# Kernel tuning notes

Hardware: AMD Instinct MI355X
Metric: run time of the kernel (lower is better)

The kernel has to match this reference:

```python
import jax, jax.numpy as jnp
import numpy as np

N_NODES = 100000
N_GRAPHS = 64
NEG_SLOPE = 0.2  # PyG GATConv default leaky_relu slope


def gat_conv(x, src, dst, W, a_src, a_dst, b, heads, out_c, concat, num_nodes):
    # x: [N, F_in]; W: [heads*out_c, F_in]; a_src/a_dst: [heads, out_c]
    h = (x @ W.T).reshape(num_nodes, heads, out_c)            # [N, H, C]
    s_src = jnp.sum(h * a_src, axis=-1)                       # [N, H]
    s_dst = jnp.sum(h * a_dst, axis=-1)                       # [N, H]
    e = jax.nn.leaky_relu(s_src[src] + s_dst[dst], NEG_SLOPE)  # [E, H]
    # segment softmax over incoming edges of each destination node
    m = jax.ops.segment_max(e, dst, num_segments=num_nodes)   # [N, H]
    m = jnp.where(jnp.isfinite(m), m, 0.0)
    e = jnp.exp(e - m[dst])
    denom = jax.ops.segment_sum(e, dst, num_segments=num_nodes)  # [N, H]
    alpha = e / (denom[dst] + 1e-16)                           # [E, H]
    msg = alpha[:, :, None] * h[src]                           # [E, H, C]
    out = jax.ops.segment_sum(msg, dst, num_segments=num_nodes)  # [N, H, C]
    if concat:
        out = out.reshape(num_nodes, heads * out_c)
    else:
        out = out.mean(axis=1)
    return out + b


def setup_inputs() -> dict:
    key = jax.random.key(0)
    ks = jax.random.split(key, 12)
    x = jax.random.normal(ks[0], (N_NODES, 128), dtype=jnp.float32)
    edge_index = jax.random.randint(ks[1], (2, 1600000), 0, N_NODES, dtype=jnp.int64)
    batch = jnp.sort(jax.random.randint(ks[2], (N_NODES,), 0, N_GRAPHS, dtype=jnp.int64))
    # conv1: 128 -> 16, heads=4, concat -> 64
    W1 = jax.random.normal(ks[3], (64, 128), dtype=jnp.float32) * 0.1
    att_src1 = jax.random.normal(ks[4], (4, 16), dtype=jnp.float32) * 0.1
    att_dst1 = jax.random.normal(ks[5], (4, 16), dtype=jnp.float32) * 0.1
    b1 = jnp.zeros((64,), dtype=jnp.float32)
    # conv2: 64 -> 10, heads=1, concat=False
    W2 = jax.random.normal(ks[6], (10, 64), dtype=jnp.float32) * 0.1
    att_src2 = jax.random.normal(ks[7], (1, 10), dtype=jnp.float32) * 0.1
    att_dst2 = jax.random.normal(ks[8], (1, 10), dtype=jnp.float32) * 0.1
    b2 = jnp.zeros((10,), dtype=jnp.float32)
    return {"x": x, "edge_index": edge_index, "batch": batch,
            "W1": W1, "att_src1": att_src1, "att_dst1": att_dst1, "b1": b1,
            "W2": W2, "att_src2": att_src2, "att_dst2": att_dst2, "b2": b2}


def reference(x, edge_index, batch, W1, att_src1, att_dst1, b1, W2, att_src2, att_dst2, b2):
    N = x.shape[0]
    # PyG GATConv adds self-loops by default
    loop = jnp.arange(N, dtype=edge_index.dtype)
    src = jnp.concatenate([edge_index[0], loop])
    dst = jnp.concatenate([edge_index[1], loop])
    # dropout layers are inactive in eval mode
    h = gat_conv(x, src, dst, W1, att_src1, att_dst1, b1, heads=4, out_c=16, concat=True, num_nodes=N)
    h = jax.nn.elu(h)
    h = gat_conv(h, src, dst, W2, att_src2, att_dst2, b2, heads=1, out_c=10, concat=False, num_nodes=N)
    # global_mean_pool over graphs in the batch
    sums = jax.ops.segment_sum(h, batch, num_segments=N_GRAPHS)
    counts = jax.ops.segment_sum(jnp.ones((N,), dtype=h.dtype), batch, num_segments=N_GRAPHS)
    pooled = sums / jnp.maximum(counts, 1.0)[:, None]
    return jax.nn.log_softmax(pooled, axis=1)
```

## Files before the change

kernel.cpp:

```cpp
#include <hip/hip_runtime.h>
#include <hip/hip_bf16.h>
#include <math.h>

#define BSHIFT 7
#define BWIDTH (1 << BSHIFT)
#define BCAP 2560
#define A3_TILE 4096

typedef float floatx2 __attribute__((ext_vector_type(2)));
typedef __attribute__((ext_vector_type(8))) short bf16x8;
typedef __attribute__((ext_vector_type(4))) float f32x4;

__device__ inline unsigned int f2bf(float f) {
    unsigned int u = __float_as_uint(f);
    return (u + 0x7FFFu + ((u >> 16) & 1u)) >> 16;
}
__device__ inline float bflo(unsigned int u) { return __uint_as_float(u << 16); }
__device__ inline float bfhi(unsigned int u) { return __uint_as_float(u & 0xFFFF0000u); }

__device__ inline void fp8x16_fma2(uint4 Wv, float we, floatx2* q) {
    floatx2 w2; w2[0] = we; w2[1] = we;
    q[0] += w2 * __builtin_amdgcn_cvt_pk_f32_fp8((int)Wv.x, false);
    q[1] += w2 * __builtin_amdgcn_cvt_pk_f32_fp8((int)Wv.x, true);
    q[2] += w2 * __builtin_amdgcn_cvt_pk_f32_fp8((int)Wv.y, false);
    q[3] += w2 * __builtin_amdgcn_cvt_pk_f32_fp8((int)Wv.y, true);
    q[4] += w2 * __builtin_amdgcn_cvt_pk_f32_fp8((int)Wv.z, false);
    q[5] += w2 * __builtin_amdgcn_cvt_pk_f32_fp8((int)Wv.z, true);
    q[6] += w2 * __builtin_amdgcn_cvt_pk_f32_fp8((int)Wv.w, false);
    q[7] += w2 * __builtin_amdgcn_cvt_pk_f32_fp8((int)Wv.w, true);
}

#define G1_BM 128

__device__ void gemm1_body(char* smem, int bid,
    const float* __restrict__ x, const float* __restrict__ W1,
    const float* __restrict__ a_src, const float* __restrict__ a_dst,
    unsigned char* __restrict__ h1f, float* __restrict__ s1s,
    float* __restrict__ s1d, int N)
{
    unsigned short (*xb)[136] = (unsigned short(*)[136])smem;
    unsigned short (*wb)[136] = (unsigned short(*)[136])(smem + 34816);
    float (*hls)[68] = (float(*)[68])smem;

    int tid = threadIdx.x;
    int nb = bid * G1_BM;

    #pragma unroll
    for (int r = 0; r < 8; ++r) {
        int i = tid + r * 256;
        int ch = i >> 5, kq = i & 31;
        float4 v = *(const float4*)&W1[ch * 128 + kq * 4];
        uint2 pk;
        pk.x = f2bf(v.x) | (f2bf(v.y) << 16);
        pk.y = f2bf(v.z) | (f2bf(v.w) << 16);
        *(uint2*)&wb[ch][kq * 4] = pk;
    }
    #pragma unroll
    for (int r = 0; r < 16; ++r) {
        int i = tid + r * 256;
        int nl = i >> 5, kq = i & 31;
        int n = nb + nl;
        float4 v = (n < N) ? *(const float4*)&x[(size_t)n * 128 + kq * 4]
                           : make_float4(0.f, 0.f, 0.f, 0.f);
        uint2 pk;
        pk.x = f2bf(v.x) | (f2bf(v.y) << 16);
        pk.y = f2bf(v.z) | (f2bf(v.w) << 16);
        *(uint2*)&xb[nl][kq * 4] = pk;
    }
    __syncthreads();

    int lane = tid & 63, wv = tid >> 6;
    int lr = lane & 15, lk = lane >> 4;
    f32x4 acc[2][4];
    #pragma unroll
    for (int mt = 0; mt < 2; ++mt)
        #pragma unroll
        for (int nt = 0; nt < 4; ++nt) acc[mt][nt] = (f32x4){0.f, 0.f, 0.f, 0.f};

    #pragma unroll
    for (int ks = 0; ks < 4; ++ks) {
        int k0 = ks * 32 + lk * 8;
        bf16x8 af0 = *(const bf16x8*)&xb[wv * 32 + lr][k0];
        bf16x8 af1 = *(const bf16x8*)&xb[wv * 32 + 16 + lr][k0];
        #pragma unroll
        for (int nt = 0; nt < 4; ++nt) {
            bf16x8 bf = *(const bf16x8*)&wb[nt * 16 + lr][k0];
            acc[0][nt] = __builtin_amdgcn_mfma_f32_16x16x32_bf16(af0, bf, acc[0][nt], 0, 0, 0);
            acc[1][nt] = __builtin_amdgcn_mfma_f32_16x16x32_bf16(af1, bf, acc[1][nt], 0, 0, 0);
        }
    }
    __syncthreads();
    #pragma unroll
    for (int mt = 0; mt < 2; ++mt)
        #pragma unroll
        for (int nt = 0; nt < 4; ++nt)
            #pragma unroll
            for (int reg = 0; reg < 4; ++reg)
                hls[wv * 32 + mt * 16 + lk * 4 + reg][nt * 16 + lr] = acc[mt][nt][reg];
    __syncthreads();

    int nl = tid >> 1, half = tid & 1;
    int n = nb + nl;
    if (n < N) {
        float v[32];
        #pragma unroll
        for (int q = 0; q < 8; ++q) {
            float4 t4 = *(const float4*)&hls[nl][half * 32 + q * 4];
            v[q*4+0] = t4.x; v[q*4+1] = t4.y; v[q*4+2] = t4.z; v[q*4+3] = t4.w;
        }
        int h0 = half * 2, h1 = half * 2 + 1;
        float ss0 = 0.f, sd0 = 0.f, ss1 = 0.f, sd1 = 0.f;
        #pragma unroll
        for (int j = 0; j < 16; ++j) {
            ss0 += v[j] * a_src[h0 * 16 + j];
            sd0 += v[j] * a_dst[h0 * 16 + j];
            ss1 += v[16 + j] * a_src[h1 * 16 + j];
            sd1 += v[16 + j] * a_dst[h1 * 16 + j];
        }
        s1s[n * 4 + h0] = ss0; s1d[n * 4 + h0] = sd0;
        s1s[n * 4 + h1] = ss1; s1d[n * 4 + h1] = sd1;

        unsigned int w0, w1v, w2v, w3v, w4v, w5v, w6v, w7v;
        w0  = (unsigned)__builtin_amdgcn_cvt_pk_fp8_f32(v[0],  v[1],  0, false);
        w0  = (unsigned)__builtin_amdgcn_cvt_pk_fp8_f32(v[2],  v[3],  (int)w0, true);
        w1v = (unsigned)__builtin_amdgcn_cvt_pk_fp8_f32(v[4],  v[5],  0, false);
        w1v = (unsigned)__builtin_amdgcn_cvt_pk_fp8_f32(v[6],  v[7],  (int)w1v, true);
        w2v = (unsigned)__builtin_amdgcn_cvt_pk_fp8_f32(v[8],  v[9],  0, false);
        w2v = (unsigned)__builtin_amdgcn_cvt_pk_fp8_f32(v[10], v[11], (int)w2v, true);
        w3v = (unsigned)__builtin_amdgcn_cvt_pk_fp8_f32(v[12], v[13], 0, false);
        w3v = (unsigned)__builtin_amdgcn_cvt_pk_fp8_f32(v[14], v[15], (int)w3v, true);
        w4v = (unsigned)__builtin_amdgcn_cvt_pk_fp8_f32(v[16], v[17], 0, false);
        w4v = (unsigned)__builtin_amdgcn_cvt_pk_fp8_f32(v[18], v[19], (int)w4v, true);
        w5v = (unsigned)__builtin_amdgcn_cvt_pk_fp8_f32(v[20], v[21], 0, false);
        w5v = (unsigned)__builtin_amdgcn_cvt_pk_fp8_f32(v[22], v[23], (int)w5v, true);
        w6v = (unsigned)__builtin_amdgcn_cvt_pk_fp8_f32(v[24], v[25], 0, false);
        w6v = (unsigned)__builtin_amdgcn_cvt_pk_fp8_f32(v[26], v[27], (int)w6v, true);
        w7v = (unsigned)__builtin_amdgcn_cvt_pk_fp8_f32(v[28], v[29], 0, false);
        w7v = (unsigned)__builtin_amdgcn_cvt_pk_fp8_f32(v[30], v[31], (int)w7v, true);
        *(uint4*)(h1f + (size_t)n * 64 + half * 32)      = make_uint4(w0, w1v, w2v, w3v);
        *(uint4*)(h1f + (size_t)n * 64 + half * 32 + 16) = make_uint4(w4v, w5v, w6v, w7v);
    }
}

__device__ void partition_body(char* smem, int bid,
    const int* __restrict__ ei, int* __restrict__ bcnt, int* __restrict__ pairs,
    int E, int NBK)
{
    int* hist       = (int*)smem;
    int* scanb      = hist + 1024;
    int* gbase      = scanb + 1024;
    int* partial    = gbase + 1024;
    int* stage_pack = partial + 256;
    int* stage_pos  = stage_pack + A3_TILE;

    int t = threadIdx.x;
    int e0 = bid * A3_TILE;
    for (int i = t; i < 1024; i += 256) hist[i] = 0;
    __syncthreads();
    int my_b[16], my_rank[16], my_pack[16];
    #pragma unroll
    for (int j = 0; j < 16; ++j) {
        int e = e0 + j * 256 + t;
        int b = -1, pack = 0, r = 0;
        if (e < E) {
            int s = ei[e], d = ei[E + e];
            b = d >> BSHIFT;
            pack = ((d & (BWIDTH - 1)) << 17) | s;
            r = atomicAdd(&hist[b], 1);
        }
        my_b[j] = b; my_pack[j] = pack; my_rank[j] = r;
    }
    __syncthreads();
    int b4 = t * 4;
    int h0 = hist[b4], h1v = hist[b4 + 1], h2v = hist[b4 + 2], h3v = hist[b4 + 3];
    int tot = h0 + h1v + h2v + h3v;
    partial[t] = tot;
    __syncthreads();
    for (int o = 1; o < 256; o <<= 1) {
        int u = (t >= o) ? partial[t - o] : 0;
        __syncthreads();
        partial[t] += u;
        __syncthreads();
    }
    int excl = partial[t] - tot;
    scanb[b4]     = excl;
    scanb[b4 + 1] = excl + h0;
    scanb[b4 + 2] = excl + h0 + h1v;
    scanb[b4 + 3] = excl + h0 + h1v + h2v;
    int nvalid = partial[255];
    for (int b = t; b < NBK; b += 256) {
        int c = hist[b];
        if (c > 0) gbase[b] = b * BCAP + atomicAdd(&bcnt[b], c);
    }
    __syncthreads();
    #pragma unroll
    for (int j = 0; j < 16; ++j) {
        int b = my_b[j];
        if (b >= 0) {
            int slot = scanb[b] + my_rank[j];
            stage_pack[slot] = my_pack[j];
            stage_pos[slot]  = gbase[b] + my_rank[j];
        }
    }
    __syncthreads();
    for (int i = t; i < nvalid; i += 256)
        pairs[stage_pos[i]] = stage_pack[i];
}

__global__ __launch_bounds__(256) void gp_kernel(
    const float* __restrict__ x, const float* __restrict__ W1,
    const float* __restrict__ a_src, const float* __restrict__ a_dst,
    unsigned char* __restrict__ h1f, float* __restrict__ s1s,
    float* __restrict__ s1d, const int* __restrict__ ei,
    int* __restrict__ bcnt, int* __restrict__ pairs,
    int N, int E, int NBK, int G1B)
{
    __shared__ __align__(16) char smem[52224];
    if ((int)blockIdx.x < G1B)
        gemm1_body(smem, blockIdx.x, x, W1, a_src, a_dst, h1f, s1s, s1d, N);
    else
        partition_body(smem, blockIdx.x - G1B, ei, bcnt, pairs, E, NBK);
}

__global__ __launch_bounds__(256) void buildcsr_kernel(
    const int* __restrict__ pairs, const int* __restrict__ bcnt,
    int* __restrict__ csr_src, int* __restrict__ meta, int N)
{
    int b = blockIdx.x;
    __shared__ int stage[BCAP];
    __shared__ int hist[BWIDTH];
    __shared__ int scn[BWIDTH];
    __shared__ int cur[BWIDTH];
    int t = threadIdx.x;
    if (t < BWIDTH) hist[t] = 0;
    __syncthreads();
    int cnt = bcnt[b];
    int base = b * BCAP;
    for (int i = t; i < cnt; i += 256) {
        int p = pairs[base + i];
        stage[i] = p;
        atomicAdd(&hist[(p >> 17) & (BWIDTH - 1)], 1);
    }
    __syncthreads();
    int v = (t < BWIDTH) ? hist[t] : 0;
    if (t < BWIDTH) scn[t] = v;
    __syncthreads();
    for (int o = 1; o < BWIDTH; o <<= 1) {
        int u = (t < BWIDTH && t >= o) ? scn[t - o] : 0;
        __syncthreads();
        if (t < BWIDTH) scn[t] += u;
        __syncthreads();
    }
    if (t < BWIDTH) {
        int excl = scn[t] - v;
        cur[t] = excl;
        int dst = b * BWIDTH + t;
        if (dst < N) meta[dst] = (excl << 16) | v;
    }
    __syncthreads();
    for (int i = t; i < cnt; i += 256) {
        int p = stage[i];
        int slot = atomicAdd(&cur[(p >> 17) & (BWIDTH - 1)], 1);
        csr_src[base + slot] = p & 0x1FFFF;
    }
}

__global__ __launch_bounds__(256) void agg1_kernel(
    const int* __restrict__ meta, const int* __restrict__ csr_src,
    const unsigned char* __restrict__ h1f, const float* __restrict__ s1s,
    const float* __restrict__ s1d, const float* __restrict__ b1,
    const float* __restrict__ W2, const float* __restrict__ as2,
    const float* __restrict__ ad2, unsigned short* __restrict__ h2p, int N)
{
    __shared__ float w2s[640];
    for (int i = threadIdx.x; i < 640; i += 256) w2s[i] = W2[i];
    __syncthreads();

    int tid = blockIdx.x * 256 + threadIdx.x;
    int n = tid >> 4, h = tid & 3, sub = (tid >> 2) & 3;
    floatx2 xq[8];
    #pragma unroll
    for (int j = 0; j < 8; ++j) { xq[j][0] = 0.f; xq[j][1] = 0.f; }
    float den = 0.f;

    if (n < N) {
        float sdst = s1d[n * 4 + h];
        if (sub == 0) {
            float s = s1s[n * 4 + h] + sdst;
            s = (s >= 0.f) ? s : 0.2f * s;
            float w = __expf(s);
            den = w;
            uint4 Wv = *(const uint4*)(h1f + ((size_t)n << 6) + (h << 4));
            fp8x16_fma2(Wv, w, xq);
        }
        int mn = meta[n];
        int row = (n >> BSHIFT) * BCAP + (mn >> 16);
        int end = row + (mn & 0xFFFF);
        int i = row + sub;
        for (; i + 4 < end; i += 8) {
            int src0 = csr_src[i];
            int src1 = csr_src[i + 4];
            uint4 W0 = *(const uint4*)(h1f + ((size_t)src0 << 6) + (h << 4));
            uint4 W1 = *(const uint4*)(h1f + ((size_t)src1 << 6) + (h << 4));
            float a0 = s1s[src0 * 4 + h];
            float a1 = s1s[src1 * 4 + h];
            float e0 = a0 + sdst; e0 = (e0 >= 0.f) ? e0 : 0.2f * e0;
            float e1 = a1 + sdst; e1 = (e1 >= 0.f) ? e1 : 0.2f * e1;
            float w0 = __expf(e0);
            float w1 = __expf(e1);
            den += w0 + w1;
            fp8x16_fma2(W0, w0, xq);
            fp8x16_fma2(W1, w1, xq);
        }
        if (i < end) {
            int src = csr_src[i];
            uint4 Wv = *(const uint4*)(h1f + ((size_t)src << 6) + (h << 4));
            float ss = s1s[src * 4 + h] + sdst;
            ss = (ss >= 0.f) ? ss : 0.2f * ss;
            float we = __expf(ss);
            den += we;
            fp8x16_fma2(Wv, we, xq);
        }
    }
    float* xl = (float*)xq;
    #pragma unroll
    for (int j = 0; j < 16; ++j) {
        xl[j] += __shfl_xor(xl[j], 4);
        xl[j] += __shfl_xor(xl[j], 8);
    }
    den += __shfl_xor(den, 4);
    den += __shfl_xor(den, 8);

    float inv = 1.f / (den + 1e-16f);
    #pragma unroll
    for (int j = 0; j < 16; ++j) {
        float v = xl[j] * inv + b1[h * 16 + j];
        xl[j] = (v > 0.f) ? v : (__expf(v) - 1.f);
    }

    int clo = sub * 3;
    int nc = (sub == 3) ? 1 : 3;
    float part[3] = {0.f, 0.f, 0.f};
    #pragma unroll
    for (int idx = 0; idx < 3; ++idx) {
        if (idx < nc) {
            const float* wr = &w2s[(clo + idx) * 64 + h * 16];
            float p = 0.f;
            #pragma unroll
            for (int j = 0; j < 16; ++j) p += xl[j] * wr[j];
            part[idx] = p;
        }
    }
    #pragma unroll
    for (int idx = 0; idx < 3; ++idx) {
        part[idx] += __shfl_xor(part[idx], 1);
        part[idx] += __shfl_xor(part[idx], 2);
    }
    float ssp = 0.f, sdp = 0.f;
    #pragma unroll
    for (int idx = 0; idx < 3; ++idx) {
        if (idx < nc) {
            ssp += part[idx] * as2[clo + idx];
            sdp += part[idx] * ad2[clo + idx];
        }
    }
    ssp += __shfl_xor(ssp, 4); ssp += __shfl_xor(ssp, 8);
    sdp += __shfl_xor(sdp, 4); sdp += __shfl_xor(sdp, 8);

    if (n < N && h == 0) {
        #pragma unroll
        for (int idx = 0; idx < 3; ++idx)
            if (idx < nc)
                h2p[(size_t)n * 16 + clo + idx] = (unsigned short)f2bf(part[idx]);
        if (sub == 3) {
            h2p[(size_t)n * 16 + 10] = (unsigned short)f2bf(ssp);
            h2p[(size_t)n * 16 + 11] = (unsigned short)f2bf(sdp);
        }
    }
}

__global__ __launch_bounds__(256) void agg2_kernel(
    const int* __restrict__ meta, const int* __restrict__ csr_src,
    const unsigned short* __restrict__ h2p, const float* __restrict__ b2,
    float* __restrict__ node_out, int N)
{
    int tid = blockIdx.x * 256 + threadIdx.x;
    int n = tid >> 3, t = tid & 7;
    if (n >= N) return;
    floatx2 aq[5];
    #pragma unroll
    for (int c = 0; c < 5; ++c) { aq[c][0] = 0.f; aq[c][1] = 0.f; }
    float den = 0.f;

    uint2 d1 = *(const uint2*)(h2p + (size_t)n * 16 + 8);
    float sdst = bfhi(d1.y);
    if (t == 0) {
        uint4 d0 = *(const uint4*)(h2p + (size_t)n * 16);
        float s = bflo(d1.y) + sdst;
        s = (s >= 0.f) ? s : 0.2f * s;
        float w = __expf(s);
        den = w;
        floatx2 w2; w2[0] = w; w2[1] = w;
        floatx2 p;
        p[0] = bflo(d0.x); p[1] = bfhi(d0.x); aq[0] += w2 * p;
        p[0] = bflo(d0.y); p[1] = bfhi(d0.y); aq[1] += w2 * p;
        p[0] = bflo(d0.z); p[1] = bfhi(d0.z); aq[2] += w2 * p;
        p[0] = bflo(d0.w); p[1] = bfhi(d0.w); aq[3] += w2 * p;
        p[0] = bflo(d1.x); p[1] = bfhi(d1.x); aq[4] += w2 * p;
    }
    int mn = meta[n];
    int row = (n >> BSHIFT) * BCAP + (mn >> 16);
    int end = row + (mn & 0xFFFF);
    int i = row + t;
    for (; i + 8 < end; i += 16) {
        int src0 = csr_src[i];
        int src1 = csr_src[i + 8];
        uint4 A0 = *(const uint4*)(h2p + (size_t)src0 * 16);
        uint2 B0 = *(const uint2*)(h2p + (size_t)src0 * 16 + 8);
        uint4 A1 = *(const uint4*)(h2p + (size_t)src1 * 16);
        uint2 B1 = *(const uint2*)(h2p + (size_t)src1 * 16 + 8);
        float e0 = bflo(B0.y) + sdst; e0 = (e0 >= 0.f) ? e0 : 0.2f * e0;
        float e1 = bflo(B1.y) + sdst; e1 = (e1 >= 0.f) ? e1 : 0.2f * e1;
        float w0 = __expf(e0);
        float w1 = __expf(e1);
        den += w0 + w1;
        floatx2 w20; w20[0] = w0; w20[1] = w0;
        floatx2 w21; w21[0] = w1; w21[1] = w1;
        floatx2 p;
        p[0] = bflo(A0.x); p[1] = bfhi(A0.x); aq[0] += w20 * p;
        p[0] = bflo(A0.y); p[1] = bfhi(A0.y); aq[1] += w20 * p;
        p[0] = bflo(A0.z); p[1] = bfhi(A0.z); aq[2] += w20 * p;
        p[0] = bflo(A0.w); p[1] = bfhi(A0.w); aq[3] += w20 * p;
        p[0] = bflo(B0.x); p[1] = bfhi(B0.x); aq[4] += w20 * p;
        p[0] = bflo(A1.x); p[1] = bfhi(A1.x); aq[0] += w21 * p;
        p[0] = bflo(A1.y); p[1] = bfhi(A1.y); aq[1] += w21 * p;
        p[0] = bflo(A1.z); p[1] = bfhi(A1.z); aq[2] += w21 * p;
        p[0] = bflo(A1.w); p[1] = bfhi(A1.w); aq[3] += w21 * p;
        p[0] = bflo(B1.x); p[1] = bfhi(B1.x); aq[4] += w21 * p;
    }
    if (i < end) {
        int src = csr_src[i];
        uint4 A0 = *(const uint4*)(h2p + (size_t)src * 16);
        uint2 B0 = *(const uint2*)(h2p + (size_t)src * 16 + 8);
        float s = bflo(B0.y) + sdst;
        s = (s >= 0.f) ? s : 0.2f * s;
        float we = __expf(s);
        den += we;
        floatx2 w2; w2[0] = we; w2[1] = we;
        floatx2 p;
        p[0] = bflo(A0.x); p[1] = bfhi(A0.x); aq[0] += w2 * p;
        p[0] = bflo(A0.y); p[1] = bfhi(A0.y); aq[1] += w2 * p;
        p[0] = bflo(A0.z); p[1] = bfhi(A0.z); aq[2] += w2 * p;
        p[0] = bflo(A0.w); p[1] = bfhi(A0.w); aq[3] += w2 * p;
        p[0] = bflo(B0.x); p[1] = bfhi(B0.x); aq[4] += w2 * p;
    }
    float* acc = (float*)aq;
    #pragma unroll
    for (int c = 0; c < 10; ++c) {
        acc[c] += __shfl_xor(acc[c], 1);
        acc[c] += __shfl_xor(acc[c], 2);
        acc[c] += __shfl_xor(acc[c], 4);
    }
    den += __shfl_xor(den, 1);
    den += __shfl_xor(den, 2);
    den += __shfl_xor(den, 4);

    if (t == 0) {
        float inv = 1.f / (den + 1e-16f);
        float* o = &node_out[(size_t)n * 12];
        *(float4*)o = make_float4(acc[0]*inv + b2[0], acc[1]*inv + b2[1],
                                  acc[2]*inv + b2[2], acc[3]*inv + b2[3]);
        *(float4*)(o + 4) = make_float4(acc[4]*inv + b2[4], acc[5]*inv + b2[5],
                                        acc[6]*inv + b2[6], acc[7]*inv + b2[7]);
        *(float2*)(o + 8) = make_float2(acc[8]*inv + b2[8], acc[9]*inv + b2[9]);
    }
}

__global__ __launch_bounds__(256) void pool_kernel(
    const float* __restrict__ node_out, const int* __restrict__ batch,
    float* __restrict__ pooled, float* __restrict__ cnt, int N)
{
    int g = blockIdx.x;
    int lo = 0, hi = N;
    while (lo < hi) { int m = (lo + hi) >> 1; if (batch[m] < g) lo = m + 1; else hi = m; }
    int s0 = lo;
    hi = N;
    while (lo < hi) { int m = (lo + hi) >> 1; if (batch[m] < g + 1) lo = m + 1; else hi = m; }
    int s1 = lo;

    float acc[10];
    #pragma unroll
    for (int c = 0; c < 10; ++c) acc[c] = 0.f;
    for (int i = s0 + threadIdx.x; i < s1; i += 256) {
        const float* o = &node_out[(size_t)i * 12];
        float4 a = *(const float4*)o;
        float4 b = *(const float4*)(o + 4);
        float2 d = *(const float2*)(o + 8);
        acc[0] += a.x; acc[1] += a.y; acc[2] += a.z; acc[3] += a.w;
        acc[4] += b.x; acc[5] += b.y; acc[6] += b.z; acc[7] += b.w;
        acc[8] += d.x; acc[9] += d.y;
    }
    #pragma unroll
    for (int c = 0; c < 10; ++c)
        for (int o = 32; o > 0; o >>= 1) acc[c] += __shfl_down(acc[c], o);
    __shared__ float part[4][10];
    int wave = threadIdx.x >> 6, lane = threadIdx.x & 63;
    if (lane == 0)
        #pragma unroll
        for (int c = 0; c < 10; ++c) part[wave][c] = acc[c];
    __syncthreads();
    if (threadIdx.x < 10) {
        float s = part[0][threadIdx.x] + part[1][threadIdx.x]
                + part[2][threadIdx.x] + part[3][threadIdx.x];
        pooled[g * 10 + threadIdx.x] = s;
        if (threadIdx.x == 0) cnt[g] = (float)(s1 - s0);
    }
}

__global__ void final_kernel(const float* __restrict__ pooled,
                             const float* __restrict__ cnt, float* __restrict__ out)
{
    int g = threadIdx.x;
    if (g >= 64) return;
    float c = cnt[g];
    if (c < 1.f) c = 1.f;
    float v[10], m = -1e30f;
    #pragma unroll
    for (int i = 0; i < 10; ++i) {
        v[i] = pooled[g * 10 + i] / c;
        m = fmaxf(m, v[i]);
    }
    float s = 0.f;
    #pragma unroll
    for (int i = 0; i < 10; ++i) s += __expf(v[i] - m);
    float lse = m + logf(s);
    #pragma unroll
    for (int i = 0; i < 10; ++i) out[g * 10 + i] = v[i] - lse;
}

extern "C" void kernel_launch(void* const* d_in, const int* in_sizes, int n_in,
                              void* d_out, int out_size, void* d_ws, size_t ws_size,
                              hipStream_t stream) {
    const float* x       = (const float*)d_in[0];
    const int*   ei      = (const int*)  d_in[1];
    const int*   batch   = (const int*)  d_in[2];
    const float* W1      = (const float*)d_in[3];
    const float* a_src1  = (const float*)d_in[4];
    const float* a_dst1  = (const float*)d_in[5];
    const float* b1      = (const float*)d_in[6];
    const float* W2      = (const float*)d_in[7];
    const float* a_src2  = (const float*)d_in[8];
    const float* a_dst2  = (const float*)d_in[9];
    const float* b2      = (const float*)d_in[10];
    float* out = (float*)d_out;

    int N = in_sizes[0] / 128;
    int E = in_sizes[1] / 2;
    int NBK = (N + BWIDTH - 1) >> BSHIFT;

    float* f = (float*)d_ws;
    size_t off = 0;
    unsigned char* h1f = (unsigned char*)(f + off);
    float* node_out = (float*)h1f;
    off += (size_t)N * 16;
    float* s1s  = f + off; off += (size_t)N * 4;
    float* s1d  = f + off; off += (size_t)N * 4;
    unsigned short* h2p = (unsigned short*)(f + off);
    int*  pairs = (int*)(f + off);
    size_t r1 = ((size_t)N * 8 > (size_t)NBK * BCAP) ? (size_t)N * 8 : (size_t)NBK * BCAP;
    off += r1;
    int* iw = (int*)(f + off);
    size_t ioff = 0;
    int* meta    = iw + ioff; ioff += (size_t)N;
    int* csr_src = iw + ioff; ioff += (size_t)NBK * BCAP;
    int* bcnt    = iw + ioff; ioff += (size_t)NBK;
    float* pooled = (float*)(iw + ioff);
    float* cnt    = pooled + 640;

    hipMemsetAsync((void*)bcnt, 0, (size_t)NBK * sizeof(int), stream);

    int g1_blocks = (N + G1_BM - 1) / G1_BM;
    int ntiles = (E + A3_TILE - 1) / A3_TILE;
    gp_kernel<<<g1_blocks + ntiles, 256, 0, stream>>>(
        x, W1, a_src1, a_dst1, h1f, s1s, s1d, ei, bcnt, pairs, N, E, NBK, g1_blocks);

    buildcsr_kernel<<<NBK, 256, 0, stream>>>(pairs, bcnt, csr_src, meta, N);

    agg1_kernel<<<(N * 16 + 255) / 256, 256, 0, stream>>>(
        meta, csr_src, h1f, s1s, s1d, b1, W2, a_src2, a_dst2, h2p, N);

    agg2_kernel<<<(N * 8 + 255) / 256, 256, 0, stream>>>(
        meta, csr_src, h2p, b2, node_out, N);

    pool_kernel<<<64, 256, 0, stream>>>(node_out, batch, pooled, cnt, N);

    final_kernel<<<1, 64, 0, stream>>>(pooled, cnt, out);
}
```

Measured before the change: 124.8 us.

## Degree-sort nodes for aggregation, pre-convert W1, interleave GEMM/partition blocks

Adds a setup kernel that zeroes bucket counts and converts W1 to bf16 once, replacing the memset and the per-block conversion. GEMM blocks now keep the W fragments in registers instead of LDS, which shrinks shared memory and adds an occupancy hint. The fused kernel interleaves GEMM and partition blocks, and the partition tile is halved. buildcsr now emits a per-bucket node order sorted by degree, which agg1 and agg2 use to cut wavefront divergence from uneven degrees. The cost is an extra indirection load and some scan work in buildcsr.

```diff
diff --git a/kernel.cpp b/kernel.cpp
--- a/kernel.cpp
+++ b/kernel.cpp
@@ -5,7 +5,7 @@
 #define BSHIFT 7
 #define BWIDTH (1 << BSHIFT)
 #define BCAP 2560
-#define A3_TILE 4096
+#define A3_TILE 2048
 
 typedef float floatx2 __attribute__((ext_vector_type(2)));
 typedef __attribute__((ext_vector_type(8))) short bf16x8;
@@ -32,29 +32,48 @@
 
 #define G1_BM 128
 
+__global__ __launch_bounds__(256) void setup_kernel(
+    int* __restrict__ bcnt, int NBK,
+    const float* __restrict__ W1, unsigned short* __restrict__ w1b)
+{
+    if (blockIdx.x == 0) {
+        for (int i = threadIdx.x; i < NBK; i += 256) bcnt[i] = 0;
+    } else {
+        int t = threadIdx.x;
+        #pragma unroll
+        for (int r = 0; r < 8; ++r) {
+            int i4 = t + r * 256;
+            int ch = i4 >> 5, kq = i4 & 31;
+            float4 v = *(const float4*)&W1[ch * 128 + kq * 4];
+            uint2 pk;
+            pk.x = f2bf(v.x) | (f2bf(v.y) << 16);
+            pk.y = f2bf(v.z) | (f2bf(v.w) << 16);
+            *(uint2*)&w1b[ch * 128 + kq * 4] = pk;
+        }
+    }
+}
+
 __device__ void gemm1_body(char* smem, int bid,
-    const float* __restrict__ x, const float* __restrict__ W1,
+    const float* __restrict__ x, const unsigned short* __restrict__ w1b,
     const float* __restrict__ a_src, const float* __restrict__ a_dst,
     unsigned char* __restrict__ h1f, float* __restrict__ s1s,
     float* __restrict__ s1d, int N)
 {
     unsigned short (*xb)[136] = (unsigned short(*)[136])smem;
-    unsigned short (*wb)[136] = (unsigned short(*)[136])(smem + 34816);
     float (*hls)[68] = (float(*)[68])smem;
 
     int tid = threadIdx.x;
     int nb = bid * G1_BM;
-
-    #pragma unroll
-    for (int r = 0; r < 8; ++r) {
-        int i = tid + r * 256;
-        int ch = i >> 5, kq = i & 31;
-        float4 v = *(const float4*)&W1[ch * 128 + kq * 4];
-        uint2 pk;
-        pk.x = f2bf(v.x) | (f2bf(v.y) << 16);
-        pk.y = f2bf(v.z) | (f2bf(v.w) << 16);
-        *(uint2*)&wb[ch][kq * 4] = pk;
-    }
+    int lane = tid & 63, wv = tid >> 6;
+    int lr = lane & 15, lk = lane >> 4;
+
+    bf16x8 Bf[4][4];
+    #pragma unroll
+    for (int ks = 0; ks < 4; ++ks)
+        #pragma unroll
+        for (int nt = 0; nt < 4; ++nt)
+            Bf[ks][nt] = *(const bf16x8*)&w1b[(nt * 16 + lr) * 128 + ks * 32 + lk * 8];
+
     #pragma unroll
     for (int r = 0; r < 16; ++r) {
         int i = tid + r * 256;
@@ -69,8 +88,6 @@
     }
     __syncthreads();
 
-    int lane = tid & 63, wv = tid >> 6;
-    int lr = lane & 15, lk = lane >> 4;
     f32x4 acc[2][4];
     #pragma unroll
     for (int mt = 0; mt < 2; ++mt)
@@ -84,9 +101,8 @@
         bf16x8 af1 = *(const bf16x8*)&xb[wv * 32 + 16 + lr][k0];
         #pragma unroll
         for (int nt = 0; nt < 4; ++nt) {
-            bf16x8 bf = *(const bf16x8*)&wb[nt * 16 + lr][k0];
-            acc[0][nt] = __builtin_amdgcn_mfma_f32_16x16x32_bf16(af0, bf, acc[0][nt], 0, 0, 0);
-            acc[1][nt] = __builtin_amdgcn_mfma_f32_16x16x32_bf16(af1, bf, acc[1][nt], 0, 0, 0);
+            acc[0][nt] = __builtin_amdgcn_mfma_f32_16x16x32_bf16(af0, Bf[ks][nt], acc[0][nt], 0, 0, 0);
+            acc[1][nt] = __builtin_amdgcn_mfma_f32_16x16x32_bf16(af1, Bf[ks][nt], acc[1][nt], 0, 0, 0);
         }
     }
     __syncthreads();
@@ -157,9 +173,9 @@
     int e0 = bid * A3_TILE;
     for (int i = t; i < 1024; i += 256) hist[i] = 0;
     __syncthreads();
-    int my_b[16], my_rank[16], my_pack[16];
-    #pragma unroll
-    for (int j = 0; j < 16; ++j) {
+    int my_b[8], my_rank[8], my_pack[8];
+    #pragma unroll
+    for (int j = 0; j < 8; ++j) {
         int e = e0 + j * 256 + t;
         int b = -1, pack = 0, r = 0;
         if (e < E) {
@@ -194,7 +210,7 @@
     }
     __syncthreads();
     #pragma unroll
-    for (int j = 0; j < 16; ++j) {
+    for (int j = 0; j < 8; ++j) {
         int b = my_b[j];
         if (b >= 0) {
             int slot = scanb[b] + my_rank[j];
@@ -207,32 +223,43 @@
         pairs[stage_pos[i]] = stage_pack[i];
 }
 
-__global__ __launch_bounds__(256) void gp_kernel(
-    const float* __restrict__ x, const float* __restrict__ W1,
+__global__ __launch_bounds__(256, 4) void gp_kernel(
+    const float* __restrict__ x, const unsigned short* __restrict__ w1b,
     const float* __restrict__ a_src, const float* __restrict__ a_dst,
     unsigned char* __restrict__ h1f, float* __restrict__ s1s,
     float* __restrict__ s1d, const int* __restrict__ ei,
     int* __restrict__ bcnt, int* __restrict__ pairs,
-    int N, int E, int NBK, int G1B)
-{
-    __shared__ __align__(16) char smem[52224];
-    if ((int)blockIdx.x < G1B)
-        gemm1_body(smem, blockIdx.x, x, W1, a_src, a_dst, h1f, s1s, s1d, N);
+    int N, int E, int NBK, int G1B, int ntiles)
+{
+    __shared__ __align__(16) char smem[34816];
+    int bid = blockIdx.x;
+    int nmin2 = 2 * ((G1B < ntiles) ? G1B : ntiles);
+    bool isg; int id;
+    if (bid < nmin2) { isg = (bid & 1) == 0; id = bid >> 1; }
+    else {
+        int r = bid - nmin2;
+        isg = (G1B > ntiles);
+        id = nmin2 / 2 + r;
+    }
+    if (isg)
+        gemm1_body(smem, id, x, w1b, a_src, a_dst, h1f, s1s, s1d, N);
     else
-        partition_body(smem, blockIdx.x - G1B, ei, bcnt, pairs, E, NBK);
+        partition_body(smem, id, ei, bcnt, pairs, E, NBK);
 }
 
 __global__ __launch_bounds__(256) void buildcsr_kernel(
     const int* __restrict__ pairs, const int* __restrict__ bcnt,
-    int* __restrict__ csr_src, int* __restrict__ meta, int N)
+    int* __restrict__ csr_src, int* __restrict__ meta, int* __restrict__ order, int N)
 {
     int b = blockIdx.x;
     __shared__ int stage[BCAP];
     __shared__ int hist[BWIDTH];
     __shared__ int scn[BWIDTH];
     __shared__ int cur[BWIDTH];
+    __shared__ int dh[64], dsc[64];
     int t = threadIdx.x;
     if (t < BWIDTH) hist[t] = 0;
+    if (t >= BWIDTH && t < BWIDTH + 64) dh[t - BWIDTH] = 0;
     __syncthreads();
     int cnt = bcnt[b];
     int base = b * BCAP;
@@ -251,11 +278,29 @@
         if (t < BWIDTH) scn[t] += u;
         __syncthreads();
     }
+    int dst = b * BWIDTH + t;
+    int bin = 63;
     if (t < BWIDTH) {
         int excl = scn[t] - v;
         cur[t] = excl;
-        int dst = b * BWIDTH + t;
         if (dst < N) meta[dst] = (excl << 16) | v;
+        bin = (dst < N) ? ((v < 62) ? v : 62) : 63;
+        atomicAdd(&dh[bin], 1);
+    }
+    __syncthreads();
+    if (t < 64) dsc[t] = dh[t];
+    __syncthreads();
+    for (int o = 1; o < 64; o <<= 1) {
+        int u = (t < 64 && t >= o) ? dsc[t - o] : 0;
+        __syncthreads();
+        if (t < 64) dsc[t] += u;
+        __syncthreads();
+    }
+    if (t < 64) dh[t] = dsc[t] - dh[t];
+    __syncthreads();
+    if (t < BWIDTH) {
+        int r = atomicAdd(&dh[bin], 1);
+        order[b * BWIDTH + r] = (dst < N) ? dst : -1;
     }
     __syncthreads();
     for (int i = t; i < cnt; i += 256) {
@@ -266,7 +311,8 @@
 }
 
 __global__ __launch_bounds__(256) void agg1_kernel(
-    const int* __restrict__ meta, const int* __restrict__ csr_src,
+    const int* __restrict__ order, const int* __restrict__ meta,
+    const int* __restrict__ csr_src,
     const unsigned char* __restrict__ h1f, const float* __restrict__ s1s,
     const float* __restrict__ s1d, const float* __restrict__ b1,
     const float* __restrict__ W2, const float* __restrict__ as2,
@@ -277,13 +323,14 @@
     __syncthreads();
 
     int tid = blockIdx.x * 256 + threadIdx.x;
-    int n = tid >> 4, h = tid & 3, sub = (tid >> 2) & 3;
+    int n = order[tid >> 4];
+    int h = tid & 3, sub = (tid >> 2) & 3;
     floatx2 xq[8];
     #pragma unroll
     for (int j = 0; j < 8; ++j) { xq[j][0] = 0.f; xq[j][1] = 0.f; }
     float den = 0.f;
 
-    if (n < N) {
+    if (n >= 0) {
         float sdst = s1d[n * 4 + h];
         if (sub == 0) {
             float s = s1s[n * 4 + h] + sdst;
@@ -367,7 +414,7 @@
     ssp += __shfl_xor(ssp, 4); ssp += __shfl_xor(ssp, 8);
     sdp += __shfl_xor(sdp, 4); sdp += __shfl_xor(sdp, 8);
 
-    if (n < N && h == 0) {
+    if (n >= 0 && h == 0) {
         #pragma unroll
         for (int idx = 0; idx < 3; ++idx)
             if (idx < nc)
@@ -380,13 +427,15 @@
 }
 
 __global__ __launch_bounds__(256) void agg2_kernel(
-    const int* __restrict__ meta, const int* __restrict__ csr_src,
+    const int* __restrict__ order, const int* __restrict__ meta,
+    const int* __restrict__ csr_src,
     const unsigned short* __restrict__ h2p, const float* __restrict__ b2,
     float* __restrict__ node_out, int N)
 {
     int tid = blockIdx.x * 256 + threadIdx.x;
-    int n = tid >> 3, t = tid & 7;
-    if (n >= N) return;
+    int n = order[tid >> 3];
+    int t = tid & 7;
+    if (n < 0) return;
     floatx2 aq[5];
     #pragma unroll
     for (int c = 0; c < 5; ++c) { aq[c][0] = 0.f; aq[c][1] = 0.f; }
@@ -565,6 +614,7 @@
     off += (size_t)N * 16;
     float* s1s  = f + off; off += (size_t)N * 4;
     float* s1d  = f + off; off += (size_t)N * 4;
+    unsigned short* w1b = (unsigned short*)(f + off); off += 4096;
     unsigned short* h2p = (unsigned short*)(f + off);
     int*  pairs = (int*)(f + off);
     size_t r1 = ((size_t)N * 8 > (size_t)NBK * BCAP) ? (size_t)N * 8 : (size_t)NBK * BCAP;
@@ -574,23 +624,26 @@
     int* meta    = iw + ioff; ioff += (size_t)N;
     int* csr_src = iw + ioff; ioff += (size_t)NBK * BCAP;
     int* bcnt    = iw + ioff; ioff += (size_t)NBK;
+    int* order   = iw + ioff; ioff += (size_t)NBK * BWIDTH;
     float* pooled = (float*)(iw + ioff);
     float* cnt    = pooled + 640;
 
-    hipMemsetAsync((void*)bcnt, 0, (size_t)NBK * sizeof(int), stream);
-
     int g1_blocks = (N + G1_BM - 1) / G1_BM;
     int ntiles = (E + A3_TILE - 1) / A3_TILE;
+
+    setup_kernel<<<2, 256, 0, stream>>>(bcnt, NBK, W1, w1b);
+
     gp_kernel<<<g1_blocks + ntiles, 256, 0, stream>>>(
-        x, W1, a_src1, a_dst1, h1f, s1s, s1d, ei, bcnt, pairs, N, E, NBK, g1_blocks);
-
-    buildcsr_kernel<<<NBK, 256, 0, stream>>>(pairs, bcnt, csr_src, meta, N);
-
-    agg1_kernel<<<(N * 16 + 255) / 256, 256, 0, stream>>>(
-        meta, csr_src, h1f, s1s, s1d, b1, W2, a_src2, a_dst2, h2p, N);
-
-    agg2_kernel<<<(N * 8 + 255) / 256, 256, 0, stream>>>(
-        meta, csr_src, h2p, b2, node_out, N);
+        x, w1b, a_src1, a_dst1, h1f, s1s, s1d, ei, bcnt, pairs,
+        N, E, NBK, g1_blocks, ntiles);
+
+    buildcsr_kernel<<<NBK, 256, 0, stream>>>(pairs, bcnt, csr_src, meta, order, N);
+
+    agg1_kernel<<<NBK * 8, 256, 0, stream>>>(
+        order, meta, csr_src, h1f, s1s, s1d, b1, W2, a_src2, a_dst2, h2p, N);
+
+    agg2_kernel<<<NBK * 4, 256, 0, stream>>>(
+        order, meta, csr_src, h2p, b2, node_out, N);
 
     pool_kernel<<<64, 256, 0, stream>>>(node_out, batch, pooled, cnt, N);
 
```

Measured after the change: 143.4 us. +14.9%, slower.
